# Kernel optimization log

Measured on AMD Instinct MI355X. Metric: run time of the kernel, lower is better.

## Reference

```python
import jax, jax.numpy as jnp
import numpy as np
from jax import lax

HW = 256 * 256      # patch h*w
WINDOW = 65536
STRIDE = 32768


def _conv2d(x, w, b, stride, pad):
    y = lax.conv_general_dilated(x, w, (stride, stride), [(pad, pad), (pad, pad)],
                                 dimension_numbers=('NCHW', 'OIHW', 'NCHW'))
    return y + b[None, :, None, None]


def _fcn(x, w1, b1, w2, b2, w3, b3, w4, b4):
    x = jax.nn.relu(_conv2d(x, w1, b1, 6, 6))
    x = jax.nn.relu(_conv2d(x, w2, b2, 4, 4))
    x = jax.nn.relu(_conv2d(x, w3, b3, 2, 2))
    x = jax.nn.relu(_conv2d(x, w4, b4, 1, 1))
    return x


def _avgpool2(x):
    # torch AvgPool2d(2,2,padding=1), count_include_pad=True -> sum window / 4
    s = lax.reduce_window(x, 0.0, lax.add, (1, 1, 2, 2), (1, 1, 2, 2),
                          [(0, 0), (0, 0), (1, 1), (1, 1)])
    return s * 0.25


def _cca(x, qw, qb, kw, kb, vw, vb, gamma):
    B, C, H, W = x.shape
    q = _conv2d(x, qw, qb, 1, 0)   # (B, C//8, H, W)
    k = _conv2d(x, kw, kb, 1, 0)
    v = _conv2d(x, vw, vb, 1, 0)   # (B, C, H, W)
    # column (height-axis) energies with -inf on the diagonal (self position)
    eH = jnp.einsum('bchw,bcgw->bhwg', q, k)                     # (B,H,W,H')
    eH = jnp.where(jnp.eye(H, dtype=bool)[:, None, :], -jnp.inf, eH)
    # row (width-axis) energies
    eW = jnp.einsum('bchw,bchv->bhwv', q, k)                     # (B,H,W,W')
    att = jax.nn.softmax(jnp.concatenate([eH, eW], axis=3), axis=3)
    outH = jnp.einsum('bcgw,bhwg->bchw', v, att[..., :H])
    outW = jnp.einsum('bchv,bhwv->bchw', v, att[..., H:])
    return gamma * (outH + outW) + x


def _forward(x, f0_w1, f0_b1, f0_w2, f0_b2, f0_w3, f0_b3, f0_w4, f0_b4,
             f1_w1, f1_b1, f1_w2, f1_b2, f1_w3, f1_b3, f1_w4, f1_b4,
             qw, qb, kw, kb, vw, vb, gamma, cls_w, cls_b):
    B, nc, L = x.shape
    need = HW - L % HW                 # torch pads a full extra block when L % hw == 0
    xp = jnp.pad(x, ((0, 0), (0, 0), (0, need)))
    nw = (L + need - WINDOW) // STRIDE + 1
    idx = jnp.arange(nw)[:, None] * STRIDE + jnp.arange(WINDOW)[None, :]
    wins = xp[:, 0, :][:, idx]                      # (B, nw, WINDOW) ~ torch unfold
    # torch does a raw reshape (nw,1,h,w) -> (1,1,h*w,nw); row-major reshape matches
    c_in = wins.reshape(B, 1, HW, nw)
    c0 = _fcn(c_in, f0_w1, f0_b1, f0_w2, f0_b2, f0_w3, f0_b3, f0_w4, f0_b4)
    c1 = _fcn(_avgpool2(c_in), f1_w1, f1_b1, f1_w2, f1_b2, f1_w3, f1_b3, f1_w4, f1_b4)
    a0 = _cca(c0, qw, qb, kw, kb, vw, vb, gamma)
    a1 = _cca(c1, qw, qb, kw, kb, vw, vb, gamma)   # 'twoheadfcn' reuses cca_attn0
    feat = jnp.concatenate([a0.mean(axis=(2, 3)), a1.mean(axis=(2, 3))], axis=1)
    return feat @ cls_w.T + cls_b                   # dropout = identity at eval


def setup_inputs():
    key = jax.random.key(0)
    ks = jax.random.split(key, 32)

    def he(k, shape):
        fan_in = int(np.prod(shape[1:]))
        return (jax.random.normal(k, shape) / np.sqrt(fan_in)).astype(jnp.float32)

    inp = {'x': jax.random.uniform(ks[0], (2, 1, 4194304), dtype=jnp.float32)}
    shapes = [(64, 1, 12, 12), (128, 64, 8, 8), (256, 128, 5, 5), (128, 256, 3, 3)]
    for pre, off in (('f0', 1), ('f1', 9)):
        for i, s in enumerate(shapes):
            inp[f'{pre}_w{i+1}'] = he(ks[off + 2 * i], s)
            inp[f'{pre}_b{i+1}'] = (0.01 * jax.random.normal(ks[off + 2 * i + 1], (s[0],))).astype(jnp.float32)
    inp['qw'] = he(ks[17], (16, 128, 1, 1)); inp['qb'] = jnp.zeros((16,), jnp.float32)
    inp['kw'] = he(ks[18], (16, 128, 1, 1)); inp['kb'] = jnp.zeros((16,), jnp.float32)
    inp['vw'] = he(ks[19], (128, 128, 1, 1)); inp['vb'] = jnp.zeros((128,), jnp.float32)
    inp['gamma'] = jnp.full((1,), 0.1, jnp.float32)
    inp['cls_w'] = he(ks[20], (2, 256)); inp['cls_b'] = jnp.zeros((2,), jnp.float32)
    return inp


def reference(x, f0_w1, f0_b1, f0_w2, f0_b2, f0_w3, f0_b3, f0_w4, f0_b4,
              f1_w1, f1_b1, f1_w2, f1_b2, f1_w3, f1_b3, f1_w4, f1_b4,
              qw, qb, kw, kb, vw, vb, gamma, cls_w, cls_b):
    return _forward(x, f0_w1, f0_b1, f0_w2, f0_b2, f0_w3, f0_b3, f0_w4, f0_b4,
                    f1_w1, f1_b1, f1_w2, f1_b2, f1_w3, f1_b3, f1_w4, f1_b4,
                    qw, qb, kw, kb, vw, vb, gamma, cls_w, cls_b)
```

## Files before the change

### kernel.cpp

```cpp
#include <hip/hip_runtime.h>
#include <math.h>

#define BLK 256
static const long LX = 4194304;

typedef __bf16 bf16x8 __attribute__((ext_vector_type(8)));
typedef float  f32x4  __attribute__((ext_vector_type(4)));
typedef unsigned short u16;

__device__ __forceinline__ void bf16split(float x, u16& h, u16& l) {
    unsigned u = __float_as_uint(x);
    unsigned hr = (u + 0x7fffu + ((u >> 16) & 1u)) >> 16;
    h = (u16)hr;
    float hf = __uint_as_float(hr << 16);
    float r = x - hf;
    unsigned v = __float_as_uint(r);
    unsigned lr2 = (v + 0x7fffu + ((v >> 16) & 1u)) >> 16;
    l = (u16)lr2;
}

__device__ __forceinline__ float cin_val(const float* __restrict__ x, long xbase, int h, int w) {
    if ((unsigned)h >= 65536u || (unsigned)w >= 129u) return 0.f;
    long flat = (long)h * 129 + w;
    int n = (int)(flat >> 16);
    int q = (int)(flat & 65535);
    long pos = (long)n * 32768 + q;
    return (pos < LX) ? x[xbase + pos] : 0.f;
}

__global__ __launch_bounds__(256)
void conv1_mfma_k(const float* __restrict__ x, const u16* __restrict__ wbh,
                  const u16* __restrict__ wbl, const float* __restrict__ bias,
                  u16* __restrict__ outh, u16* __restrict__ outl) {
    const long SPT = 240306;
    __shared__ u16 ph[6400];
    __shared__ u16 pl[6400];
    const int tid = threadIdx.x;
    const int b = blockIdx.y;
    const long sp0 = (long)blockIdx.x * 128;
    const long xbase = (long)b * LX;
    const int ho_min = (int)sp0 / 22;
    const int flat_start = (ho_min * 6 - 6) * 129 - 6;
    for (int i = tid; i < 6400; i += 256) {
        int flat = flat_start + i;
        float v = 0.f;
        if (flat >= 0 && flat < 65536 * 129) {
            int n = flat >> 16, q = flat & 65535;
            long pos = (long)n * 32768 + q;
            if (pos < LX) v = x[xbase + pos];
        }
        u16 h, l; bf16split(v, h, l);
        ph[i] = h; pl[i] = l;
    }
    __syncthreads();

    const int lane = tid & 63, wid = tid >> 6;
    const int lr = lane & 15;
    const int lk = (lane >> 4) << 3;

    int off0[2]; int wlo[2], whi[2];
#pragma unroll
    for (int fm = 0; fm < 2; fm++) {
        int r = (wid << 5) + (fm << 4) + lr;
        long spl = sp0 + r; if (spl >= SPT) spl = SPT - 1;
        int sp = (int)spl;
        int ho = sp / 22;
        int wo = sp - ho * 22;
        off0[fm] = (ho * 6 - 6) * 129 + (wo * 6 - 6) - flat_start;
        wlo[fm] = (wo == 0) ? 1 : 0;
        whi[fm] = (wo == 21) ? 1 : 0;
    }

    f32x4 acc[2][4];
#pragma unroll
    for (int fn = 0; fn < 4; fn++) {
        float bv = bias[(fn << 4) + lr];
#pragma unroll
        for (int fm = 0; fm < 2; fm++) { f32x4 v = {bv, bv, bv, bv}; acc[fm][fn] = v; }
    }

    const bool zhi = (lk >= 16);
#pragma unroll
    for (int c = 0; c < 5; c++) {
        bf16x8 bH[4], bL[4];
#pragma unroll
        for (int fn = 0; fn < 4; fn++) {
            int oc = (fn << 4) + lr;
            bH[fn] = *(const bf16x8*)(wbh + oc * 160 + (c << 5) + lk);
            bL[fn] = *(const bf16x8*)(wbl + oc * 160 + (c << 5) + lk);
        }
        bf16x8 aH[2], aL[2];
#pragma unroll
        for (int fm = 0; fm < 2; fm++) {
            union { bf16x8 v; u16 u[8]; } uh, ul;
            if (c == 4 && zhi) {
#pragma unroll
                for (int jj = 0; jj < 8; jj++) { uh.u[jj] = 0; ul.u[jj] = 0; }
            } else {
                int t0 = (c << 5) + lk;
                int kh0 = t0 / 12;
                int r0 = t0 - kh0 * 12;
                int jst = 12 - r0;
                int base = off0[fm] + t0 + kh0 * 117;
#pragma unroll
                for (int jj = 0; jj < 8; jj++) {
                    int wrapped = (jj >= jst) ? 1 : 0;
                    int idx = base + jj + (wrapped ? 117 : 0);
                    int kw = r0 + jj - (wrapped ? 12 : 0);
                    int bad = (wlo[fm] & ((kw < 6) ? 1 : 0)) | (whi[fm] & ((kw > 8) ? 1 : 0));
                    u16 hv = ph[idx];
                    u16 lv = pl[idx];
                    uh.u[jj] = bad ? (u16)0 : hv;
                    ul.u[jj] = bad ? (u16)0 : lv;
                }
            }
            aH[fm] = uh.v; aL[fm] = ul.v;
        }
#pragma unroll
        for (int fm = 0; fm < 2; fm++)
#pragma unroll
            for (int fn = 0; fn < 4; fn++) {
                acc[fm][fn] = __builtin_amdgcn_mfma_f32_16x16x32_bf16(aL[fm], bH[fn], acc[fm][fn], 0, 0, 0);
                acc[fm][fn] = __builtin_amdgcn_mfma_f32_16x16x32_bf16(aH[fm], bL[fn], acc[fm][fn], 0, 0, 0);
                acc[fm][fn] = __builtin_amdgcn_mfma_f32_16x16x32_bf16(aH[fm], bH[fn], acc[fm][fn], 0, 0, 0);
            }
    }
    const int row0 = (lane >> 4) << 2;
#pragma unroll
    for (int fm = 0; fm < 2; fm++) {
#pragma unroll
        for (int q = 0; q < 4; q++) {
            long sp = sp0 + (wid << 5) + (fm << 4) + row0 + q;
            if (sp < SPT) {
                long obase = ((long)b * SPT + sp) << 6;
#pragma unroll
                for (int fn = 0; fn < 4; fn++) {
                    u16 h, l;
                    bf16split(fmaxf(acc[fm][fn][q], 0.f), h, l);
                    outh[obase + (fn << 4) + lr] = h;
                    outl[obase + (fn << 4) + lr] = l;
                }
            }
        }
    }
}

__global__ __launch_bounds__(BLK)
void reorder_w1m_k(const float* __restrict__ w, u16* __restrict__ wh, u16* __restrict__ wl) {
    int t = blockIdx.x * BLK + threadIdx.x;
    if (t >= 64 * 160) return;
    int tap = t % 160, oc = t / 160;
    float v = (tap < 144) ? w[oc * 144 + tap] : 0.f;
    u16 h, l; bf16split(v, h, l);
    wh[t] = h; wl[t] = l;
}

template<int TOC>
__global__ __launch_bounds__(BLK)
void conv1_plane_k(const float* __restrict__ in, const float* __restrict__ wr1,
                   const float* __restrict__ bias, u16* __restrict__ outh, u16* __restrict__ outl,
                   int B, int Hin, int Win, int Cout, int Hout, int Wout) {
    const int K = 12, S = 6, P = 6;
    long spatial = (long)B * Hout * Wout;
    long idx = (long)blockIdx.x * BLK + threadIdx.x;
    if (idx >= spatial) return;
    int wo = (int)(idx % Wout);
    long t = idx / Wout;
    int ho = (int)(t % Hout);
    int b  = (int)(t / Hout);
    int oc0 = blockIdx.y * TOC;
    float acc[TOC];
#pragma unroll
    for (int i = 0; i < TOC; i++) acc[i] = bias[oc0 + i];
    const float* inb = in + (long)b * Hin * Win;
    int h0 = ho * S - P, w0 = wo * S - P;
    for (int kh = 0; kh < K; kh++) {
        int h = h0 + kh;
        bool hok = (unsigned)h < (unsigned)Hin;
        const float* row = inb + (long)h * Win;
        for (int kw = 0; kw < K; kw++) {
            int w = w0 + kw;
            float v = (hok && (unsigned)w < (unsigned)Win) ? row[w] : 0.f;
            const float* wp = wr1 + (kh * K + kw) * Cout + oc0;
#pragma unroll
            for (int i = 0; i < TOC; i++) acc[i] = fmaf(v, wp[i], acc[i]);
        }
    }
    u16* oph = outh + idx * Cout + oc0;
    u16* opl = outl + idx * Cout + oc0;
#pragma unroll
    for (int i4 = 0; i4 < TOC / 4; i4++) {
        u16 hx, hy, hz, hw2, la, lb, lc, ld;
        bf16split(fmaxf(acc[i4*4+0], 0.f), hx, la);
        bf16split(fmaxf(acc[i4*4+1], 0.f), hy, lb);
        bf16split(fmaxf(acc[i4*4+2], 0.f), hz, lc);
        bf16split(fmaxf(acc[i4*4+3], 0.f), hw2, ld);
        *(ushort4*)(oph + i4 * 4) = make_ushort4(hx, hy, hz, hw2);
        *(ushort4*)(opl + i4 * 4) = make_ushort4(la, lb, lc, ld);
    }
}

__global__ __launch_bounds__(BLK)
void avgpool_synth_k(const float* __restrict__ x, float* __restrict__ out, int B) {
    const int Ho = 32769, Wo = 65;
    long total = (long)B * Ho * Wo;
    long idx = (long)blockIdx.x * BLK + threadIdx.x;
    if (idx >= total) return;
    int w2 = (int)(idx % Wo);
    long t = idx / Wo;
    int p2 = (int)(t % Ho);
    int b  = (int)(t / Ho);
    long xbase = (long)b * LX;
    float s = 0.f;
#pragma unroll
    for (int dh = 0; dh < 2; dh++)
#pragma unroll
        for (int dw = 0; dw < 2; dw++)
            s += cin_val(x, xbase, 2 * p2 - 1 + dh, 2 * w2 - 1 + dw);
    out[idx] = 0.25f * s;
}

__global__ __launch_bounds__(BLK)
void reorder_w_k(const float* __restrict__ w, float* __restrict__ wrT,
                 int Cout, int Cin, int K2) {
    long total = (long)Cout * Cin * K2;
    long t = (long)blockIdx.x * BLK + threadIdx.x;
    if (t >= total) return;
    int khw = (int)(t % K2);
    long r = t / K2;
    int ic = (int)(r % Cin);
    int oc = (int)(r / Cin);
    wrT[((long)khw * Cin + ic) * Cout + oc] = w[t];
}

__global__ __launch_bounds__(BLK)
void reorder_ws_k(const float* __restrict__ w, u16* __restrict__ wh, u16* __restrict__ wl,
                  int Cout, int Cin, int Kk) {
    long total = (long)Cout * Cin * Kk * Kk;
    long t = (long)blockIdx.x * BLK + threadIdx.x;
    if (t >= total) return;
    int kw = (int)(t % Kk);
    long r = t / Kk;
    int kh = (int)(r % Kk); r /= Kk;
    int ic = (int)(r % Cin);
    int oc = (int)(r / Cin);
    long dst = (long)oc * (Cin * Kk * Kk) + (long)(kh * Kk + kw) * Cin + ic;
    u16 h, l; bf16split(w[t], h, l);
    wh[dst] = h; wl[dst] = l;
}

struct MJob {
    const u16* Ah; const u16* Al; const u16* Wh; const u16* Wl;
    const float* bias; float* out; float* part;
    int Hin, Win, Cin, cshift, Cout, K, S, P, Hout, Wout, relu, nks;
    long total; int nbx; int Ktot;
};

__global__ __launch_bounds__(256)
void mgemm2_k(MJob j0, MJob j1, int split) {
    __shared__ u16 lds[2][4][128 * 32];
    MJob j = j0;
    int bid = blockIdx.x;
    if (bid >= split) { j = j1; bid -= split; }
    const int bx = bid % j.nbx;
    int r2 = bid / j.nbx;
    const int nocb = j.Cout >> 7;
    const int ocb = (r2 % nocb) << 7;
    const int ks  = r2 / nocb;
    const int tid = threadIdx.x;
    const long spbase = (long)bx * 128;
    const int nchunk = j.Ktot >> 5;
    const int cbeg = (ks * nchunk) / j.nks;
    const int cend = ((ks + 1) * nchunk) / j.nks;

    const int sr = tid >> 1;
    const int sh = (tid & 1) << 4;
    long ssp = spbase + sr;
    const bool sval = ssp < j.total;
    long tt = sval ? ssp : 0;
    const int swo = (int)(tt % j.Wout); tt /= j.Wout;
    const int sho = (int)(tt % j.Hout);
    const int sb  = (int)(tt / j.Hout);
    const int sh0 = sho * j.S - j.P, sw0 = swo * j.S - j.P;
    const long ibase = (long)sb * j.Hin * j.Win;
    const long wbase = (long)(ocb + sr) * j.Ktot + sh;
    const int so = sr * 32 + sh;

    uint4 rA0, rA1, rL0, rL1, rB0, rB1, rM0, rM1;
    auto fetch = [&](int c) {
        int p0 = c << 5;
        int khw = p0 >> j.cshift;
        int ic0 = p0 - (khw << j.cshift);
        int kh = khw / j.K, kw = khw - kh * j.K;
        int h = sh0 + kh, w = sw0 + kw;
        bool ok = sval && (unsigned)h < (unsigned)j.Hin && (unsigned)w < (unsigned)j.Win;
        uint4 z = make_uint4(0u, 0u, 0u, 0u);
        const long e = (ibase + (long)h * j.Win + w) * j.Cin + ic0 + sh;
        rA0 = ok ? *(const uint4*)(j.Ah + e)     : z;
        rA1 = ok ? *(const uint4*)(j.Ah + e + 8) : z;
        rL0 = ok ? *(const uint4*)(j.Al + e)     : z;
        rL1 = ok ? *(const uint4*)(j.Al + e + 8) : z;
        const long we = wbase + p0;
        rB0 = *(const uint4*)(j.Wh + we);
        rB1 = *(const uint4*)(j.Wh + we + 8);
        rM0 = *(const uint4*)(j.Wl + we);
        rM1 = *(const uint4*)(j.Wl + we + 8);
    };
    auto store = [&](int buf) {
        *(uint4*)&lds[buf][0][so] = rA0; *(uint4*)&lds[buf][0][so + 8] = rA1;
        *(uint4*)&lds[buf][1][so] = rL0; *(uint4*)&lds[buf][1][so + 8] = rL1;
        *(uint4*)&lds[buf][2][so] = rB0; *(uint4*)&lds[buf][2][so + 8] = rB1;
        *(uint4*)&lds[buf][3][so] = rM0; *(uint4*)&lds[buf][3][so + 8] = rM1;
    };

    const int lane = tid & 63;
    const int wid = tid >> 6;
    const int wm = (wid >> 1) << 6, wn = (wid & 1) << 6;
    const int lr = lane & 15;
    const int lk = (lane >> 4) << 3;

    f32x4 acc[4][4];
    if (j.nks == 1) {
#pragma unroll
        for (int fn = 0; fn < 4; fn++) {
            float b = j.bias[ocb + wn + fn * 16 + lr];
#pragma unroll
            for (int fm = 0; fm < 4; fm++) { f32x4 v = {b, b, b, b}; acc[fm][fn] = v; }
        }
    } else {
#pragma unroll
        for (int fm = 0; fm < 4; fm++)
#pragma unroll
            for (int fn = 0; fn < 4; fn++) { f32x4 v = {0.f, 0.f, 0.f, 0.f}; acc[fm][fn] = v; }
    }

    fetch(cbeg); store(0);
    __syncthreads();

    for (int c = cbeg; c < cend; c++) {
        const int cur = (c - cbeg) & 1, nxt = cur ^ 1;
        const bool more = (c + 1 < cend);
        if (more) fetch(c + 1);
        const u16* Ahs = &lds[cur][0][0];
        const u16* Als = &lds[cur][1][0];
        const u16* Bhs = &lds[cur][2][0];
        const u16* Bls = &lds[cur][3][0];
        bf16x8 aH[4], aL[4], bH[4], bL[4];
#pragma unroll
        for (int f = 0; f < 4; f++) {
            aH[f] = *(const bf16x8*)(Ahs + (wm + f * 16 + lr) * 32 + lk);
            aL[f] = *(const bf16x8*)(Als + (wm + f * 16 + lr) * 32 + lk);
            bH[f] = *(const bf16x8*)(Bhs + (wn + f * 16 + lr) * 32 + lk);
            bL[f] = *(const bf16x8*)(Bls + (wn + f * 16 + lr) * 32 + lk);
        }
#pragma unroll
        for (int fm = 0; fm < 4; fm++)
#pragma unroll
            for (int fn = 0; fn < 4; fn++) {
                acc[fm][fn] = __builtin_amdgcn_mfma_f32_16x16x32_bf16(aL[fm], bH[fn], acc[fm][fn], 0, 0, 0);
                acc[fm][fn] = __builtin_amdgcn_mfma_f32_16x16x32_bf16(aH[fm], bL[fn], acc[fm][fn], 0, 0, 0);
                acc[fm][fn] = __builtin_amdgcn_mfma_f32_16x16x32_bf16(aH[fm], bH[fn], acc[fm][fn], 0, 0, 0);
            }
        if (more) store(nxt);
        __syncthreads();
    }

    const int row0 = (lane >> 4) << 2;
    if (j.nks == 1) {
#pragma unroll
        for (int fm = 0; fm < 4; fm++) {
#pragma unroll
            for (int q = 0; q < 4; q++) {
                long sp = spbase + wm + fm * 16 + row0 + q;
                if (sp < j.total) {
                    float* op = j.out + sp * j.Cout + ocb + wn + lr;
#pragma unroll
                    for (int fn = 0; fn < 4; fn++) {
                        float v = acc[fm][fn][q];
                        if (j.relu) v = fmaxf(v, 0.f);
                        op[fn * 16] = v;
                    }
                }
            }
        }
    } else {
        float* pb = j.part + ((long)ks * j.total) * j.Cout;
#pragma unroll
        for (int fm = 0; fm < 4; fm++) {
#pragma unroll
            for (int q = 0; q < 4; q++) {
                long sp = spbase + wm + fm * 16 + row0 + q;
                if (sp < j.total) {
                    float* op = pb + sp * j.Cout + ocb + wn + lr;
#pragma unroll
                    for (int fn = 0; fn < 4; fn++) op[fn * 16] = acc[fm][fn][q];
                }
            }
        }
    }
}

struct CJob {
    const float* part; const float* bias;
    float* outf; u16* outh; u16* outl;
    long n; int C; int nks; int relu;
};

__global__ __launch_bounds__(BLK)
void combine2m_k(CJob a, CJob b) {
    long q0 = a.n * (long)a.C / 4, q1 = b.n * (long)b.C / 4;
    long id = (long)blockIdx.x * BLK + threadIdx.x;
    CJob j; long f4;
    if (id < q0) { j = a; f4 = id * 4; }
    else if (id < q0 + q1) { j = b; f4 = (id - q0) * 4; }
    else return;
    long stride = j.n * (long)j.C;
    int cb = (int)(f4 % j.C);
    float4 s = *(const float4*)(j.bias + cb);
    for (int ss = 0; ss < j.nks; ss++) {
        float4 p = *(const float4*)(j.part + ss * stride + f4);
        s.x += p.x; s.y += p.y; s.z += p.z; s.w += p.w;
    }
    if (j.relu) {
        s.x = fmaxf(s.x, 0.f); s.y = fmaxf(s.y, 0.f);
        s.z = fmaxf(s.z, 0.f); s.w = fmaxf(s.w, 0.f);
    }
    if (j.outf) *(float4*)(j.outf + f4) = s;
    if (j.outh) {
        u16 hx, hy, hz, hw2, la, lb, lc, ld;
        bf16split(s.x, hx, la); bf16split(s.y, hy, lb);
        bf16split(s.z, hz, lc); bf16split(s.w, hw2, ld);
        *(ushort4*)(j.outh + f4) = make_ushort4(hx, hy, hz, hw2);
        *(ushort4*)(j.outl + f4) = make_ushort4(la, lb, lc, ld);
    }
}

__global__ __launch_bounds__(256)
void qk2_k(const float* __restrict__ in,
           const float* __restrict__ qw, const float* __restrict__ qb,
           const float* __restrict__ kw2, const float* __restrict__ kb2,
           float* __restrict__ outq, float* __restrict__ outk, long total) {
    const float* w    = blockIdx.y ? kw2 : qw;
    const float* bias = blockIdx.y ? kb2 : qb;
    float* out        = blockIdx.y ? outk : outq;
    __shared__ float As[64 * 132];
    __shared__ float Ws[128 * 16];
    int tid = threadIdx.x;
    long spbase = (long)blockIdx.x * 64;
    int r = tid >> 2;
    int cpart = (tid & 3) << 5;
    long sp = spbase + r;
    bool ok = sp < total;
    const float* ip = in + sp * 128 + cpart;
#pragma unroll
    for (int jj = 0; jj < 8; jj++) {
        float4 v = ok ? *(const float4*)(ip + jj * 4) : make_float4(0.f, 0.f, 0.f, 0.f);
        *(float4*)&As[r * 132 + cpart + jj * 4] = v;
    }
    for (int t = tid; t < 2048; t += 256) Ws[(t & 127) * 16 + (t >> 7)] = w[t];
    __syncthreads();
    int ocp = (tid & 3) << 2;
    float acc[4] = {bias[ocp], bias[ocp + 1], bias[ocp + 2], bias[ocp + 3]};
    for (int ic = 0; ic < 128; ic++) {
        float a = As[r * 132 + ic];
#pragma unroll
        for (int jj = 0; jj < 4; jj++) acc[jj] = fmaf(a, Ws[ic * 16 + ocp + jj], acc[jj]);
    }
    if (ok) {
#pragma unroll
        for (int jj = 0; jj < 4; jj++) out[sp * 16 + ocp + jj] = acc[jj];
    }
}

struct AJob {
    const float* q; const float* kk; const float* v;
    float* pacc; float* pm; float* pl;
    int B, H, W, nrt, ns, ntile;
};

__global__ __launch_bounds__(256)
void cca_part_k(AJob j0, AJob j1, int n0) {
    const int RT = 16, TG = 64;
    __shared__ float lbuf[8192];
    __shared__ float mlb2[32];
    float* kls    = lbuf;
    float* sc     = lbuf + 1088;
    float* scales = lbuf + 2176;
    AJob j = j0;
    int bid = blockIdx.x;
    if (bid >= n0) { j = j1; bid -= n0; }
    int rt = bid % j.nrt; int t = bid / j.nrt;
    int ksp = t % j.ns; t /= j.ns;
    int w = t % j.W; int b = t / j.W;
    const int H = j.H, W = j.W;
    const int tid = threadIdx.x;
    const int r = tid >> 4, l16 = tid & 15;
    const int h = rt * RT + r;
    const int hc = (h < H) ? h : (H - 1);
    const long colbase = (long)b * H * W + w;
    const long rowbase = ((long)b * H + hc) * W;

    float qreg[16];
    {
        const float* qp = j.q + (rowbase + w) * 16;
#pragma unroll
        for (int jj = 0; jj < 4; jj++) {
            float4 t4 = *(const float4*)(qp + 4 * jj);
            qreg[4*jj] = t4.x; qreg[4*jj+1] = t4.y; qreg[4*jj+2] = t4.z; qreg[4*jj+3] = t4.w;
        }
    }
    const int lane6 = tid & 63;
    const int wid = tid >> 6;
    const int c2 = lane6 << 1;
    float accv[16][2];
#pragma unroll
    for (int i = 0; i < 16; i++) { accv[i][0] = 0.f; accv[i][1] = 0.f; }

    float m = -INFINITY, l = 0.f;
    const int gp = l16 * 4;

    const int tbeg = (ksp * j.ntile) / j.ns;
    const int tend = ((ksp + 1) * j.ntile) / j.ns;
    for (int tt2 = tbeg; tt2 < tend; tt2++) {
        const int g0 = tt2 * TG;
        {
            int kr = tid >> 2, kc = (tid & 3) << 2;
            int gg = g0 + kr;
            float4 kv = make_float4(0.f, 0.f, 0.f, 0.f);
            if (gg < H) kv = *(const float4*)(j.kk + (colbase + (long)gg * W) * 16 + kc);
            kls[kr * 17 + kc + 0] = kv.x; kls[kr * 17 + kc + 1] = kv.y;
            kls[kr * 17 + kc + 2] = kv.z; kls[kr * 17 + kc + 3] = kv.w;
        }
        __syncthreads();
        float sloc[4];
#pragma unroll
        for (int i = 0; i < 4; i++) {
            int gg = g0 + gp + i;
            float d = 0.f;
#pragma unroll
            for (int c = 0; c < 16; c++) d = fmaf(qreg[c], kls[(gp + i) * 17 + c], d);
            sloc[i] = (gg >= H || gg == h) ? -INFINITY : d;
        }
        float tmax = fmaxf(fmaxf(sloc[0], sloc[1]), fmaxf(sloc[2], sloc[3]));
#pragma unroll
        for (int off = 1; off < 16; off <<= 1) tmax = fmaxf(tmax, __shfl_xor(tmax, off, 16));
        float mt = fmaxf(m, tmax);
        float scale = __expf(m - mt);
        float ps = 0.f;
#pragma unroll
        for (int i = 0; i < 4; i++) {
            float p = __expf(sloc[i] - mt);
            ps += p;
            sc[r * 68 + gp + i] = p;
        }
#pragma unroll
        for (int off = 1; off < 16; off <<= 1) ps += __shfl_xor(ps, off, 16);
        l = l * scale + ps;
        m = mt;
        if (l16 == 0) scales[r] = scale;
        __syncthreads();
        {
            float4 sA = *(const float4*)&scales[0];
            float4 sB = *(const float4*)&scales[4];
            float4 sC = *(const float4*)&scales[8];
            float4 sD = *(const float4*)&scales[12];
            float sarr[16] = {sA.x,sA.y,sA.z,sA.w, sB.x,sB.y,sB.z,sB.w,
                              sC.x,sC.y,sC.z,sC.w, sD.x,sD.y,sD.z,sD.w};
#pragma unroll
            for (int row = 0; row < 16; row++) {
                accv[row][0] *= sarr[row];
                accv[row][1] *= sarr[row];
            }
#pragma unroll
            for (int s = 0; s < 2; s++) {
                const int k0 = (wid << 4) + (s << 3);
                float2 v2[8];
#pragma unroll
                for (int kq = 0; kq < 8; kq++) {
                    int gg = g0 + k0 + kq;
                    if (gg >= H) gg = H - 1;
                    v2[kq] = *(const float2*)(j.v + (colbase + (long)gg * W) * 128 + c2);
                }
#pragma unroll
                for (int row = 0; row < 16; row++) {
                    float4 pA = *(const float4*)&sc[row * 68 + k0];
                    float4 pB = *(const float4*)&sc[row * 68 + k0 + 4];
                    accv[row][0] = fmaf(pA.x, v2[0].x, accv[row][0]);
                    accv[row][1] = fmaf(pA.x, v2[0].y, accv[row][1]);
                    accv[row][0] = fmaf(pA.y, v2[1].x, accv[row][0]);
                    accv[row][1] = fmaf(pA.y, v2[1].y, accv[row][1]);
                    accv[row][0] = fmaf(pA.z, v2[2].x, accv[row][0]);
                    accv[row][1] = fmaf(pA.z, v2[2].y, accv[row][1]);
                    accv[row][0] = fmaf(pA.w, v2[3].x, accv[row][0]);
                    accv[row][1] = fmaf(pA.w, v2[3].y, accv[row][1]);
                    accv[row][0] = fmaf(pB.x, v2[4].x, accv[row][0]);
                    accv[row][1] = fmaf(pB.x, v2[4].y, accv[row][1]);
                    accv[row][0] = fmaf(pB.y, v2[5].x, accv[row][0]);
                    accv[row][1] = fmaf(pB.y, v2[5].y, accv[row][1]);
                    accv[row][0] = fmaf(pB.z, v2[6].x, accv[row][0]);
                    accv[row][1] = fmaf(pB.z, v2[6].y, accv[row][1]);
                    accv[row][0] = fmaf(pB.w, v2[7].x, accv[row][0]);
                    accv[row][1] = fmaf(pB.w, v2[7].y, accv[row][1]);
                }
            }
        }
        __syncthreads();
    }
    if (ksp == 0) {
        float sw[3];
        float twmax = -INFINITY;
#pragma unroll
        for (int jj = 0; jj < 3; jj++) {
            sw[jj] = -INFINITY;
            if (jj < W) {
                const float* kp = j.kk + (rowbase + jj) * 16;
                float d = 0.f;
#pragma unroll
                for (int c = 0; c < 16; c++) d = fmaf(qreg[c], kp[c], d);
                sw[jj] = d;
                twmax = fmaxf(twmax, d);
            }
        }
        float mt = fmaxf(m, twmax);
        float scale = __expf(m - mt);
        l *= scale;
#pragma unroll
        for (int jj = 0; jj < 3; jj++) {
            if (jj < W) {
                float p = __expf(sw[jj] - mt);
                l += p;
                if (l16 == 0) sc[r * 68 + jj] = p;
            }
        }
        m = mt;
        if (l16 == 0) scales[r] = scale;
    }
    if (l16 == 0) { mlb2[2 * r] = m; mlb2[2 * r + 1] = l; }
    __syncthreads();
    if (ksp == 0) {
        float4 sA = *(const float4*)&scales[0];
        float4 sB = *(const float4*)&scales[4];
        float4 sC = *(const float4*)&scales[8];
        float4 sD = *(const float4*)&scales[12];
        float sarr[16] = {sA.x,sA.y,sA.z,sA.w, sB.x,sB.y,sB.z,sB.w,
                          sC.x,sC.y,sC.z,sC.w, sD.x,sD.y,sD.z,sD.w};
#pragma unroll
        for (int row = 0; row < 16; row++) {
            accv[row][0] *= sarr[row];
            accv[row][1] *= sarr[row];
            int hr = rt * RT + row;
            int hcr = (hr < H) ? hr : (H - 1);
            long rb = ((long)b * H + hcr) * W;
#pragma unroll
            for (int jj = 0; jj < 3; jj++) {
                if (jj < W) {
                    float p = sc[row * 68 + jj];
                    float2 vv = *(const float2*)(j.v + (rb + jj) * 128 + c2);
                    accv[row][0] = fmaf(p, vv.x, accv[row][0]);
                    accv[row][1] = fmaf(p, vv.y, accv[row][1]);
                }
            }
        }
    }
    __syncthreads();
#pragma unroll
    for (int row = 0; row < 16; row++) {
        *(float2*)&lbuf[(wid << 11) + (row << 7) + c2] = make_float2(accv[row][0], accv[row][1]);
    }
    __syncthreads();
    {
        int orow = tid >> 4, ocb = (tid & 15) << 3;
        int hr = rt * RT + orow;
        if (hr < H) {
            float4 r0 = make_float4(0.f, 0.f, 0.f, 0.f);
            float4 r1 = make_float4(0.f, 0.f, 0.f, 0.f);
#pragma unroll
            for (int wv = 0; wv < 4; wv++) {
                float4 a0 = *(const float4*)&lbuf[(wv << 11) + (orow << 7) + ocb];
                float4 a1 = *(const float4*)&lbuf[(wv << 11) + (orow << 7) + ocb + 4];
                r0.x += a0.x; r0.y += a0.y; r0.z += a0.z; r0.w += a0.w;
                r1.x += a1.x; r1.y += a1.y; r1.z += a1.z; r1.w += a1.w;
            }
            long qi = ((long)b * H + hr) * W + w;
            float* pp = j.pacc + (qi * j.ns + ksp) * 128 + ocb;
            *(float4*)pp       = r0;
            *(float4*)(pp + 4) = r1;
            if ((tid & 15) == 0) {
                j.pm[qi * j.ns + ksp] = mlb2[2 * orow];
                j.pl[qi * j.ns + ksp] = mlb2[2 * orow + 1];
            }
        }
    }
}

struct CCJob {
    const float* x; const float* pacc; const float* pm; const float* pl;
    float* out; long rows; int ns;
};

__global__ __launch_bounds__(BLK)
void cca_comb_k(CCJob a, CCJob b, const float* __restrict__ gamma) {
    long q0 = a.rows * 32, q1 = b.rows * 32;
    long id = (long)blockIdx.x * BLK + threadIdx.x;
    CCJob j; long lid;
    if (id < q0) { j = a; lid = id; }
    else if (id < q0 + q1) { j = b; lid = id - q0; }
    else return;
    long qi = lid >> 5;
    int c4 = (int)(lid & 31) << 2;
    int ns = j.ns;
    float M = -INFINITY;
    for (int s = 0; s < ns; s++) M = fmaxf(M, j.pm[qi * ns + s]);
    float L = 0.f;
    float4 acc = make_float4(0.f, 0.f, 0.f, 0.f);
    for (int s = 0; s < ns; s++) {
        float wgt = __expf(j.pm[qi * ns + s] - M);
        L += j.pl[qi * ns + s] * wgt;
        float4 p = *(const float4*)(j.pacc + (qi * ns + s) * 128 + c4);
        acc.x = fmaf(wgt, p.x, acc.x); acc.y = fmaf(wgt, p.y, acc.y);
        acc.z = fmaf(wgt, p.z, acc.z); acc.w = fmaf(wgt, p.w, acc.w);
    }
    float g = gamma[0] / L;
    float4 xr = *(const float4*)(j.x + qi * 128 + c4);
    float4 o = make_float4(g * acc.x + xr.x, g * acc.y + xr.y,
                           g * acc.z + xr.z, g * acc.w + xr.w);
    *(float4*)(j.out + qi * 128 + c4) = o;
}

__global__ __launch_bounds__(BLK)
void mean_part_k(const float* __restrict__ a, float* __restrict__ part, int HW, int NS) {
    int bx = blockIdx.x;
    int b = bx / NS, sc_ = bx % NS;
    int tid = threadIdx.x;
    int c = tid & 127, half = tid >> 7;
    int per = (HW + NS - 1) / NS;
    int s0 = sc_ * per, s1 = s0 + per; if (s1 > HW) s1 = HW;
    float acc = 0.f;
    for (int s = s0 + half; s < s1; s += 2) acc += a[((long)b * HW + s) * 128 + c];
    __shared__ float red[BLK];
    red[tid] = acc; __syncthreads();
    if (half == 0) part[(long)bx * 128 + c] = red[c] + red[c + 128];
}

__global__ __launch_bounds__(BLK)
void final2_k(const float* __restrict__ part0, const float* __restrict__ part1, int NS,
              const float* __restrict__ w, const float* __restrict__ bias,
              float* __restrict__ out, float hw0, float hw1) {
    __shared__ float feat[512];
    int tid = threadIdx.x;
    for (int t = tid; t < 512; t += BLK) {
        int b = t >> 8, c = t & 255;
        float s = 0.f;
        if (c < 128) {
            for (int ns = 0; ns < NS; ns++) s += part0[((long)b * NS + ns) * 128 + c];
            s /= hw0;
        } else {
            int cc = c - 128;
            for (int ns = 0; ns < NS; ns++) s += part1[((long)b * NS + ns) * 128 + cc];
            s /= hw1;
        }
        feat[t] = s;
    }
    __syncthreads();
    if (tid < 4) {
        int b = tid >> 1, jj = tid & 1;
        float s = bias[jj];
        for (int c = 0; c < 256; c++) s += feat[b * 256 + c] * w[jj * 256 + c];
        out[b * 2 + jj] = s;
    }
}

static inline long cdiv(long a, long b) { return (a + b - 1) / b; }

extern "C" void kernel_launch(void* const* d_in, const int* in_sizes, int n_in,
                              void* d_out, int out_size, void* d_ws, size_t ws_size,
                              hipStream_t stream) {
    const float* x     = (const float*)d_in[0];
    const float* f0w1  = (const float*)d_in[1];
    const float* f0b1  = (const float*)d_in[2];
    const float* f0w2  = (const float*)d_in[3];
    const float* f0b2  = (const float*)d_in[4];
    const float* f0w3  = (const float*)d_in[5];
    const float* f0b3  = (const float*)d_in[6];
    const float* f0w4  = (const float*)d_in[7];
    const float* f0b4  = (const float*)d_in[8];
    const float* f1w1  = (const float*)d_in[9];
    const float* f1b1  = (const float*)d_in[10];
    const float* f1w2  = (const float*)d_in[11];
    const float* f1b2  = (const float*)d_in[12];
    const float* f1w3  = (const float*)d_in[13];
    const float* f1b3  = (const float*)d_in[14];
    const float* f1w4  = (const float*)d_in[15];
    const float* f1b4  = (const float*)d_in[16];
    const float* qw    = (const float*)d_in[17];
    const float* qb    = (const float*)d_in[18];
    const float* kw    = (const float*)d_in[19];
    const float* kb    = (const float*)d_in[20];
    const float* vw    = (const float*)d_in[21];
    const float* vb    = (const float*)d_in[22];
    const float* gamma = (const float*)d_in[23];
    const float* clsw  = (const float*)d_in[24];
    const float* clsb  = (const float*)d_in[25];
    float* ws = (float*)d_ws;
    float* outp = (float*)d_out;

    const int B = 2;
    size_t off = 0;
    auto alloc = [&](size_t nfl) { size_t o = off; off += (nfl + 63) & ~(size_t)63; return o; };
    size_t o_pool = alloc((size_t)B * 32769 * 65);
    size_t o_A0h  = alloc((size_t)B * 10923 * 22 * 32);
    size_t o_A0l  = alloc((size_t)B * 10923 * 22 * 32);
    size_t o_A1h  = alloc((size_t)B * 5462 * 11 * 32);
    size_t o_A1l  = alloc((size_t)B * 5462 * 11 * 32);
    size_t o_B0h  = alloc((size_t)B * 2731 * 6 * 64);
    size_t o_B0l  = alloc((size_t)B * 2731 * 6 * 64);
    size_t o_c0   = alloc((size_t)B * 1366 * 3 * 128);
    size_t o_c1   = alloc((size_t)B * 683 * 2 * 128);
    size_t o_w1r1 = alloc((size_t)144 * 64);
    size_t o_w1mh = alloc((size_t)64 * 160 / 2);
    size_t o_w1ml = alloc((size_t)64 * 160 / 2);
    size_t o_w2h0 = alloc((size_t)128 * 4096 / 2);
    size_t o_w2l0 = alloc((size_t)128 * 4096 / 2);
    size_t o_w2h1 = alloc((size_t)128 * 4096 / 2);
    size_t o_w2l1 = alloc((size_t)128 * 4096 / 2);
    size_t o_w3h0 = alloc((size_t)256 * 3200 / 2);
    size_t o_w3l0 = alloc((size_t)256 * 3200 / 2);
    size_t o_w3h1 = alloc((size_t)256 * 3200 / 2);
    size_t o_w3l1 = alloc((size_t)256 * 3200 / 2);
    size_t o_w4h0 = alloc((size_t)128 * 2304 / 2);
    size_t o_w4l0 = alloc((size_t)128 * 2304 / 2);
    size_t o_w4h1 = alloc((size_t)128 * 2304 / 2);
    size_t o_w4l1 = alloc((size_t)128 * 2304 / 2);
    size_t o_wvh  = alloc((size_t)128 * 128 / 2);
    size_t o_wvl  = alloc((size_t)128 * 128 / 2);
    size_t o_part = alloc((size_t)2 * (32772 + 8196) * 128);
    size_t need_main = off;
    size_t o_B1h = o_pool;
    size_t o_B1l = o_pool + (size_t)B * 1366 * 3 * 64;
    size_t sub = o_A0h;
    auto salloc = [&](size_t nfl) { size_t o = sub; sub += (nfl + 63) & ~(size_t)63; return o; };
    size_t o_C0h = salloc((size_t)B * 1366 * 3 * 128);
    size_t o_C0l = salloc((size_t)B * 1366 * 3 * 128);
    size_t o_C1h = salloc((size_t)B * 683 * 2 * 128);
    size_t o_C1l = salloc((size_t)B * 683 * 2 * 128);
    size_t o_c0h = salloc((size_t)B * 1366 * 3 * 64);
    size_t o_c0l = salloc((size_t)B * 1366 * 3 * 64);
    size_t o_c1h = salloc((size_t)B * 683 * 2 * 64);
    size_t o_c1l = salloc((size_t)B * 683 * 2 * 64);
    size_t o_q0  = salloc((size_t)B * 1366 * 3 * 16);
    size_t o_k0  = salloc((size_t)B * 1366 * 3 * 16);
    size_t o_v0  = salloc((size_t)B * 1366 * 3 * 128);
    size_t o_a0  = salloc((size_t)B * 1366 * 3 * 128);
    size_t o_q1  = salloc((size_t)B * 683 * 2 * 16);
    size_t o_k1  = salloc((size_t)B * 683 * 2 * 16);
    size_t o_v1  = salloc((size_t)B * 683 * 2 * 128);
    size_t o_a1  = salloc((size_t)B * 683 * 2 * 128);
    size_t o_p0  = salloc((size_t)B * 8 * 128);
    size_t o_p1  = salloc((size_t)B * 8 * 128);
    if (ws_size < need_main * sizeof(float)) {
        hipMemsetAsync(d_out, 0, (size_t)out_size * sizeof(float), stream);
        return;
    }
    auto U16 = [&](size_t o) { return (u16*)(ws + o); };

    {
        long tot = (long)B * 32769 * 65;
        avgpool_synth_k<<<dim3(cdiv(tot, BLK)), BLK, 0, stream>>>(x, ws + o_pool, B);
    }
    reorder_w_k<<<dim3(cdiv((long)64 * 144, BLK)), BLK, 0, stream>>>(f1w1, ws + o_w1r1, 64, 1, 144);
    reorder_w1m_k<<<dim3(cdiv((long)64 * 160, BLK)), BLK, 0, stream>>>(f0w1, U16(o_w1mh), U16(o_w1ml));
    reorder_ws_k<<<dim3(cdiv((long)128 * 64 * 64, BLK)), BLK, 0, stream>>>(f0w2, U16(o_w2h0), U16(o_w2l0), 128, 64, 8);
    reorder_ws_k<<<dim3(cdiv((long)128 * 64 * 64, BLK)), BLK, 0, stream>>>(f1w2, U16(o_w2h1), U16(o_w2l1), 128, 64, 8);
    reorder_ws_k<<<dim3(cdiv((long)256 * 128 * 25, BLK)), BLK, 0, stream>>>(f0w3, U16(o_w3h0), U16(o_w3l0), 256, 128, 5);
    reorder_ws_k<<<dim3(cdiv((long)256 * 128 * 25, BLK)), BLK, 0, stream>>>(f1w3, U16(o_w3h1), U16(o_w3l1), 256, 128, 5);
    reorder_ws_k<<<dim3(cdiv((long)128 * 256 * 9, BLK)), BLK, 0, stream>>>(f0w4, U16(o_w4h0), U16(o_w4l0), 128, 256, 3);
    reorder_ws_k<<<dim3(cdiv((long)128 * 256 * 9, BLK)), BLK, 0, stream>>>(f1w4, U16(o_w4h1), U16(o_w4l1), 128, 256, 3);
    reorder_ws_k<<<dim3(cdiv((long)128 * 128, BLK)), BLK, 0, stream>>>(vw, U16(o_wvh), U16(o_wvl), 128, 128, 1);
    {
        long sp = (long)B * 5462 * 11;
        conv1_plane_k<32><<<dim3(cdiv(sp, BLK), 2), BLK, 0, stream>>>(
            ws + o_pool, ws + o_w1r1, f1b1, U16(o_A1h), U16(o_A1l), B, 32769, 65, 64, 5462, 11);
    }
    {
        int nbx = (int)cdiv(240306L, 128);
        conv1_mfma_k<<<dim3(nbx, B), 256, 0, stream>>>(
            x, U16(o_w1mh), U16(o_w1ml), f0b1, U16(o_A0h), U16(o_A0l));
    }

    float* partp = ws + o_part;
    auto mkM = [&](size_t ah, size_t al, size_t wh, size_t wl, const float* bias, float* out,
                   int Hin, int Win, int Cin, int cshift, int Cout,
                   int K, int S, int P, int Hout, int Wout, int relu) {
        MJob g;
        g.Ah = U16(ah); g.Al = U16(al); g.Wh = U16(wh); g.Wl = U16(wl);
        g.bias = bias; g.out = out; g.part = nullptr;
        g.Hin = Hin; g.Win = Win; g.Cin = Cin; g.cshift = cshift; g.Cout = Cout;
        g.K = K; g.S = S; g.P = P; g.Hout = Hout; g.Wout = Wout; g.relu = relu; g.nks = 1;
        g.total = (long)B * Hout * Wout;
        g.nbx = (int)((g.total + 127) / 128);
        g.Ktot = K * K * Cin;
        return g;
    };
    auto launchM = [&](MJob a, MJob b, int nks) {
        a.nks = nks; b.nks = nks;
        a.part = partp;
        b.part = partp + (size_t)nks * a.total * a.Cout;
        int na = a.nbx * (a.Cout >> 7) * nks;
        int nb = b.nbx * (b.Cout >> 7) * nks;
        mgemm2_k<<<dim3(na + nb), 256, 0, stream>>>(a, b, na);
    };

    {
        MJob a = mkM(o_A0h, o_A0l, o_w2h0, o_w2l0, f0b2, nullptr, 10923, 22, 64, 6, 128, 8, 4, 4, 2731, 6, 1);
        MJob b = mkM(o_A1h, o_A1l, o_w2h1, o_w2l1, f1b2, nullptr, 5462, 11, 64, 6, 128, 8, 4, 4, 1366, 3, 1);
        launchM(a, b, 2);
        CJob ca = {partp, f0b2, nullptr, U16(o_B0h), U16(o_B0l), a.total, 128, 2, 1};
        CJob cb = {partp + (size_t)2 * a.total * 128, f1b2, nullptr, U16(o_B1h), U16(o_B1l), b.total, 128, 2, 1};
        long n4 = (a.total * 128 + b.total * 128) / 4;
        combine2m_k<<<dim3(cdiv(n4, BLK)), BLK, 0, stream>>>(ca, cb);
    }
    {
        MJob a = mkM(o_B0h, o_B0l, o_w3h0, o_w3l0, f0b3, nullptr, 2731, 6, 128, 7, 256, 5, 2, 2, 1366, 3, 1);
        MJob b = mkM(o_B1h, o_B1l, o_w3h1, o_w3l1, f1b3, nullptr, 1366, 3, 128, 7, 256, 5, 2, 2, 683, 2, 1);
        launchM(a, b, 3);
        CJob ca = {partp, f0b3, nullptr, U16(o_C0h), U16(o_C0l), a.total, 256, 3, 1};
        CJob cb = {partp + (size_t)3 * a.total * 256, f1b3, nullptr, U16(o_C1h), U16(o_C1l), b.total, 256, 3, 1};
        long n4 = (a.total * 256 + b.total * 256) / 4;
        combine2m_k<<<dim3(cdiv(n4, BLK)), BLK, 0, stream>>>(ca, cb);
    }
    {
        MJob a = mkM(o_C0h, o_C0l, o_w4h0, o_w4l0, f0b4, nullptr, 1366, 3, 256, 8, 128, 3, 1, 1, 1366, 3, 1);
        MJob b = mkM(o_C1h, o_C1l, o_w4h1, o_w4l1, f1b4, nullptr, 683, 2, 256, 8, 128, 3, 1, 1, 683, 2, 1);
        launchM(a, b, 6);
        CJob ca = {partp, f0b4, ws + o_c0, U16(o_c0h), U16(o_c0l), a.total, 128, 6, 1};
        CJob cb = {partp + (size_t)6 * a.total * 128, f1b4, ws + o_c1, U16(o_c1h), U16(o_c1l), b.total, 128, 6, 1};
        long n4 = (a.total * 128 + b.total * 128) / 4;
        combine2m_k<<<dim3(cdiv(n4, BLK)), BLK, 0, stream>>>(ca, cb);
    }
    {
        long tot0 = (long)B * 1366 * 3;
        qk2_k<<<dim3(cdiv(tot0, 64), 2), 256, 0, stream>>>(
            ws + o_c0, qw, qb, kw, kb, ws + o_q0, ws + o_k0, tot0);
        long tot1 = (long)B * 683 * 2;
        qk2_k<<<dim3(cdiv(tot1, 64), 2), 256, 0, stream>>>(
            ws + o_c1, qw, qb, kw, kb, ws + o_q1, ws + o_k1, tot1);
    }
    {
        MJob a = mkM(o_c0h, o_c0l, o_wvh, o_wvl, vb, ws + o_v0, 1366, 3, 128, 7, 128, 1, 1, 0, 1366, 3, 0);
        MJob b = mkM(o_c1h, o_c1l, o_wvh, o_wvl, vb, ws + o_v1, 683, 2, 128, 7, 128, 1, 1, 0, 683, 2, 0);
        launchM(a, b, 1);
    }
    {
        const int nrt0 = 86, nrt1 = 43;
        const int ns0 = 6, ns1 = 3;
        const long rows0 = (long)B * 1366 * 3;
        const long rows1 = (long)B * 683 * 2;
        size_t pp = o_part;
        auto palloc = [&](size_t nfl) { size_t o = pp; pp += (nfl + 63) & ~(size_t)63; return o; };
        size_t o_pa0 = palloc((size_t)rows0 * ns0 * 128);
        size_t o_pm0 = palloc((size_t)rows0 * ns0);
        size_t o_pl0 = palloc((size_t)rows0 * ns0);
        size_t o_pa1 = palloc((size_t)rows1 * ns1 * 128);
        size_t o_pm1 = palloc((size_t)rows1 * ns1);
        size_t o_pl1 = palloc((size_t)rows1 * ns1);
        AJob a0 = { ws + o_q0, ws + o_k0, ws + o_v0,
                    ws + o_pa0, ws + o_pm0, ws + o_pl0, B, 1366, 3, nrt0, ns0, 22 };
        AJob a1 = { ws + o_q1, ws + o_k1, ws + o_v1,
                    ws + o_pa1, ws + o_pm1, ws + o_pl1, B, 683, 2, nrt1, ns1, 11 };
        int n0 = B * 3 * nrt0 * ns0;
        int n1 = B * 2 * nrt1 * ns1;
        cca_part_k<<<dim3(n0 + n1), 256, 0, stream>>>(a0, a1, n0);
        CCJob c0 = { ws + o_c0, ws + o_pa0, ws + o_pm0, ws + o_pl0, ws + o_a0, rows0, ns0 };
        CCJob c1 = { ws + o_c1, ws + o_pa1, ws + o_pm1, ws + o_pl1, ws + o_a1, rows1, ns1 };
        long tot = (rows0 + rows1) * 32;
        cca_comb_k<<<dim3(cdiv(tot, BLK)), BLK, 0, stream>>>(c0, c1, gamma);
    }
    mean_part_k<<<dim3(B * 8), BLK, 0, stream>>>(ws + o_a0, ws + o_p0, 1366 * 3, 8);
    mean_part_k<<<dim3(B * 8), BLK, 0, stream>>>(ws + o_a1, ws + o_p1, 683 * 2, 8);
    final2_k<<<dim3(1), BLK, 0, stream>>>(ws + o_p0, ws + o_p1, 8, clsw, clsb, outp,
                                          (float)(1366 * 3), (float)(683 * 2));
}
```

Before: 748.5 us.

## Move pooled-branch conv1 to MFMA and stream GEMM weights from global

Replaces the scalar FP32 first convolution of the pooled branch with an MFMA kernel. The kernel stages a strip of the pooled input into LDS as bf16 hi/lo pairs and uses split-bf16 products, reusing the padded weight layout of the other conv1. Separately, the shared GEMM kernel no longer stages weight tiles in LDS. Each wave loads its B fragments straight from global memory, which halves LDS usage and cuts LDS traffic but relies on cache hits for weight reuse across waves.

```diff
diff --git a/kernel.cpp b/kernel.cpp
--- a/kernel.cpp
+++ b/kernel.cpp
@@ -145,6 +145,119 @@
     }
 }
 
+__global__ __launch_bounds__(256)
+void conv1p_mfma_k(const float* __restrict__ pool, const u16* __restrict__ wbh,
+                   const u16* __restrict__ wbl, const float* __restrict__ bias,
+                   u16* __restrict__ outh, u16* __restrict__ outl) {
+    const int SPT = 60082;
+    const int HWP = 32769 * 65;
+    __shared__ u16 ph[5504];
+    __shared__ u16 pl[5504];
+    const int tid = threadIdx.x;
+    const int b = blockIdx.y;
+    const long sp0 = (long)blockIdx.x * 128;
+    const float* pb = pool + (long)b * HWP;
+    const int ho_min = (int)sp0 / 11;
+    const int fs = (ho_min * 6 - 6) * 65 - 6;
+    for (int i = tid; i < 5504; i += 256) {
+        int flat = fs + i;
+        float v = (flat >= 0 && flat < HWP) ? pb[flat] : 0.f;
+        u16 h, l; bf16split(v, h, l);
+        ph[i] = h; pl[i] = l;
+    }
+    __syncthreads();
+
+    const int lane = tid & 63, wid = tid >> 6;
+    const int lr = lane & 15;
+    const int lk = (lane >> 4) << 3;
+
+    int off0[2]; int wlo[2], whi[2];
+#pragma unroll
+    for (int fm = 0; fm < 2; fm++) {
+        int r = (wid << 5) + (fm << 4) + lr;
+        long spl = sp0 + r; if (spl >= SPT) spl = SPT - 1;
+        int sp = (int)spl;
+        int ho = sp / 11;
+        int wo = sp - ho * 11;
+        off0[fm] = (ho - ho_min) * 390 + wo * 6;
+        wlo[fm] = (wo == 0) ? 1 : 0;
+        whi[fm] = (wo == 10) ? 1 : 0;
+    }
+
+    f32x4 acc[2][4];
+#pragma unroll
+    for (int fn = 0; fn < 4; fn++) {
+        float bv = bias[(fn << 4) + lr];
+#pragma unroll
+        for (int fm = 0; fm < 2; fm++) { f32x4 v = {bv, bv, bv, bv}; acc[fm][fn] = v; }
+    }
+
+    const bool zhi = (lk >= 16);
+#pragma unroll
+    for (int c = 0; c < 5; c++) {
+        bf16x8 bH[4], bL[4];
+#pragma unroll
+        for (int fn = 0; fn < 4; fn++) {
+            int oc = (fn << 4) + lr;
+            bH[fn] = *(const bf16x8*)(wbh + oc * 160 + (c << 5) + lk);
+            bL[fn] = *(const bf16x8*)(wbl + oc * 160 + (c << 5) + lk);
+        }
+        bf16x8 aH[2], aL[2];
+#pragma unroll
+        for (int fm = 0; fm < 2; fm++) {
+            union { bf16x8 v; u16 u[8]; } uh, ul;
+            if (c == 4 && zhi) {
+#pragma unroll
+                for (int jj = 0; jj < 8; jj++) { uh.u[jj] = 0; ul.u[jj] = 0; }
+            } else {
+                int t0 = (c << 5) + lk;
+                int kh0 = t0 / 12;
+                int r0 = t0 - kh0 * 12;
+                int jst = 12 - r0;
+                int base = off0[fm] + kh0 * 65 + r0;
+#pragma unroll
+                for (int jj = 0; jj < 8; jj++) {
+                    int wrapped = (jj >= jst) ? 1 : 0;
+                    int idx = base + jj + (wrapped ? 53 : 0);
+                    int kw = r0 + jj - (wrapped ? 12 : 0);
+                    int bad = (wlo[fm] & ((kw < 6) ? 1 : 0)) | (whi[fm] & ((kw > 10) ? 1 : 0));
+                    u16 hv = ph[idx];
+                    u16 lv = pl[idx];
+                    uh.u[jj] = bad ? (u16)0 : hv;
+                    ul.u[jj] = bad ? (u16)0 : lv;
+                }
+            }
+            aH[fm] = uh.v; aL[fm] = ul.v;
+        }
+#pragma unroll
+        for (int fm = 0; fm < 2; fm++)
+#pragma unroll
+            for (int fn = 0; fn < 4; fn++) {
+                acc[fm][fn] = __builtin_amdgcn_mfma_f32_16x16x32_bf16(aL[fm], bH[fn], acc[fm][fn], 0, 0, 0);
+                acc[fm][fn] = __builtin_amdgcn_mfma_f32_16x16x32_bf16(aH[fm], bL[fn], acc[fm][fn], 0, 0, 0);
+                acc[fm][fn] = __builtin_amdgcn_mfma_f32_16x16x32_bf16(aH[fm], bH[fn], acc[fm][fn], 0, 0, 0);
+            }
+    }
+    const int row0 = (lane >> 4) << 2;
+#pragma unroll
+    for (int fm = 0; fm < 2; fm++) {
+#pragma unroll
+        for (int q = 0; q < 4; q++) {
+            long sp = sp0 + (wid << 5) + (fm << 4) + row0 + q;
+            if (sp < SPT) {
+                long obase = ((long)b * SPT + sp) << 6;
+#pragma unroll
+                for (int fn = 0; fn < 4; fn++) {
+                    u16 h, l;
+                    bf16split(fmaxf(acc[fm][fn][q], 0.f), h, l);
+                    outh[obase + (fn << 4) + lr] = h;
+                    outl[obase + (fn << 4) + lr] = l;
+                }
+            }
+        }
+    }
+}
+
 __global__ __launch_bounds__(BLK)
 void reorder_w1m_k(const float* __restrict__ w, u16* __restrict__ wh, u16* __restrict__ wl) {
     int t = blockIdx.x * BLK + threadIdx.x;
@@ -153,51 +266,6 @@
     float v = (tap < 144) ? w[oc * 144 + tap] : 0.f;
     u16 h, l; bf16split(v, h, l);
     wh[t] = h; wl[t] = l;
-}
-
-template<int TOC>
-__global__ __launch_bounds__(BLK)
-void conv1_plane_k(const float* __restrict__ in, const float* __restrict__ wr1,
-                   const float* __restrict__ bias, u16* __restrict__ outh, u16* __restrict__ outl,
-                   int B, int Hin, int Win, int Cout, int Hout, int Wout) {
-    const int K = 12, S = 6, P = 6;
-    long spatial = (long)B * Hout * Wout;
-    long idx = (long)blockIdx.x * BLK + threadIdx.x;
-    if (idx >= spatial) return;
-    int wo = (int)(idx % Wout);
-    long t = idx / Wout;
-    int ho = (int)(t % Hout);
-    int b  = (int)(t / Hout);
-    int oc0 = blockIdx.y * TOC;
-    float acc[TOC];
-#pragma unroll
-    for (int i = 0; i < TOC; i++) acc[i] = bias[oc0 + i];
-    const float* inb = in + (long)b * Hin * Win;
-    int h0 = ho * S - P, w0 = wo * S - P;
-    for (int kh = 0; kh < K; kh++) {
-        int h = h0 + kh;
-        bool hok = (unsigned)h < (unsigned)Hin;
-        const float* row = inb + (long)h * Win;
-        for (int kw = 0; kw < K; kw++) {
-            int w = w0 + kw;
-            float v = (hok && (unsigned)w < (unsigned)Win) ? row[w] : 0.f;
-            const float* wp = wr1 + (kh * K + kw) * Cout + oc0;
-#pragma unroll
-            for (int i = 0; i < TOC; i++) acc[i] = fmaf(v, wp[i], acc[i]);
-        }
-    }
-    u16* oph = outh + idx * Cout + oc0;
-    u16* opl = outl + idx * Cout + oc0;
-#pragma unroll
-    for (int i4 = 0; i4 < TOC / 4; i4++) {
-        u16 hx, hy, hz, hw2, la, lb, lc, ld;
-        bf16split(fmaxf(acc[i4*4+0], 0.f), hx, la);
-        bf16split(fmaxf(acc[i4*4+1], 0.f), hy, lb);
-        bf16split(fmaxf(acc[i4*4+2], 0.f), hz, lc);
-        bf16split(fmaxf(acc[i4*4+3], 0.f), hw2, ld);
-        *(ushort4*)(oph + i4 * 4) = make_ushort4(hx, hy, hz, hw2);
-        *(ushort4*)(opl + i4 * 4) = make_ushort4(la, lb, lc, ld);
-    }
 }
 
 __global__ __launch_bounds__(BLK)
@@ -218,19 +286,6 @@
         for (int dw = 0; dw < 2; dw++)
             s += cin_val(x, xbase, 2 * p2 - 1 + dh, 2 * w2 - 1 + dw);
     out[idx] = 0.25f * s;
-}
-
-__global__ __launch_bounds__(BLK)
-void reorder_w_k(const float* __restrict__ w, float* __restrict__ wrT,
-                 int Cout, int Cin, int K2) {
-    long total = (long)Cout * Cin * K2;
-    long t = (long)blockIdx.x * BLK + threadIdx.x;
-    if (t >= total) return;
-    int khw = (int)(t % K2);
-    long r = t / K2;
-    int ic = (int)(r % Cin);
-    int oc = (int)(r / Cin);
-    wrT[((long)khw * Cin + ic) * Cout + oc] = w[t];
 }
 
 __global__ __launch_bounds__(BLK)
@@ -258,7 +313,7 @@
 
 __global__ __launch_bounds__(256)
 void mgemm2_k(MJob j0, MJob j1, int split) {
-    __shared__ u16 lds[2][4][128 * 32];
+    __shared__ u16 lds[2][2][128 * 32];
     MJob j = j0;
     int bid = blockIdx.x;
     if (bid >= split) { j = j1; bid -= split; }
@@ -283,11 +338,10 @@
     const int sb  = (int)(tt / j.Hout);
     const int sh0 = sho * j.S - j.P, sw0 = swo * j.S - j.P;
     const long ibase = (long)sb * j.Hin * j.Win;
-    const long wbase = (long)(ocb + sr) * j.Ktot + sh;
     const int so = sr * 32 + sh;
 
-    uint4 rA0, rA1, rL0, rL1, rB0, rB1, rM0, rM1;
-    auto fetch = [&](int c) {
+    uint4 rA0, rA1, rL0, rL1;
+    auto fetchA = [&](int c) {
         int p0 = c << 5;
         int khw = p0 >> j.cshift;
         int ic0 = p0 - (khw << j.cshift);
@@ -300,17 +354,10 @@
         rA1 = ok ? *(const uint4*)(j.Ah + e + 8) : z;
         rL0 = ok ? *(const uint4*)(j.Al + e)     : z;
         rL1 = ok ? *(const uint4*)(j.Al + e + 8) : z;
-        const long we = wbase + p0;
-        rB0 = *(const uint4*)(j.Wh + we);
-        rB1 = *(const uint4*)(j.Wh + we + 8);
-        rM0 = *(const uint4*)(j.Wl + we);
-        rM1 = *(const uint4*)(j.Wl + we + 8);
     };
-    auto store = [&](int buf) {
+    auto storeA = [&](int buf) {
         *(uint4*)&lds[buf][0][so] = rA0; *(uint4*)&lds[buf][0][so + 8] = rA1;
         *(uint4*)&lds[buf][1][so] = rL0; *(uint4*)&lds[buf][1][so + 8] = rL1;
-        *(uint4*)&lds[buf][2][so] = rB0; *(uint4*)&lds[buf][2][so + 8] = rB1;
-        *(uint4*)&lds[buf][3][so] = rM0; *(uint4*)&lds[buf][3][so + 8] = rM1;
     };
 
     const int lane = tid & 63;
@@ -318,6 +365,7 @@
     const int wm = (wid >> 1) << 6, wn = (wid & 1) << 6;
     const int lr = lane & 15;
     const int lk = (lane >> 4) << 3;
+    const long wrow = (long)(ocb + wn + lr) * j.Ktot + lk;
 
     f32x4 acc[4][4];
     if (j.nks == 1) {
@@ -334,24 +382,27 @@
             for (int fn = 0; fn < 4; fn++) { f32x4 v = {0.f, 0.f, 0.f, 0.f}; acc[fm][fn] = v; }
     }
 
-    fetch(cbeg); store(0);
+    fetchA(cbeg); storeA(0);
     __syncthreads();
 
     for (int c = cbeg; c < cend; c++) {
         const int cur = (c - cbeg) & 1, nxt = cur ^ 1;
         const bool more = (c + 1 < cend);
-        if (more) fetch(c + 1);
+        if (more) fetchA(c + 1);
+        bf16x8 bH[4], bL[4];
+#pragma unroll
+        for (int fn = 0; fn < 4; fn++) {
+            const long wo2 = wrow + (long)fn * 16 * j.Ktot + (c << 5);
+            bH[fn] = *(const bf16x8*)(j.Wh + wo2);
+            bL[fn] = *(const bf16x8*)(j.Wl + wo2);
+        }
         const u16* Ahs = &lds[cur][0][0];
         const u16* Als = &lds[cur][1][0];
-        const u16* Bhs = &lds[cur][2][0];
-        const u16* Bls = &lds[cur][3][0];
-        bf16x8 aH[4], aL[4], bH[4], bL[4];
+        bf16x8 aH[4], aL[4];
 #pragma unroll
         for (int f = 0; f < 4; f++) {
             aH[f] = *(const bf16x8*)(Ahs + (wm + f * 16 + lr) * 32 + lk);
             aL[f] = *(const bf16x8*)(Als + (wm + f * 16 + lr) * 32 + lk);
-            bH[f] = *(const bf16x8*)(Bhs + (wn + f * 16 + lr) * 32 + lk);
-            bL[f] = *(const bf16x8*)(Bls + (wn + f * 16 + lr) * 32 + lk);
         }
 #pragma unroll
         for (int fm = 0; fm < 4; fm++)
@@ -361,7 +412,7 @@
                 acc[fm][fn] = __builtin_amdgcn_mfma_f32_16x16x32_bf16(aH[fm], bL[fn], acc[fm][fn], 0, 0, 0);
                 acc[fm][fn] = __builtin_amdgcn_mfma_f32_16x16x32_bf16(aH[fm], bH[fn], acc[fm][fn], 0, 0, 0);
             }
-        if (more) store(nxt);
+        if (more) storeA(nxt);
         __syncthreads();
     }
 
@@ -816,9 +867,10 @@
     size_t o_B0l  = alloc((size_t)B * 2731 * 6 * 64);
     size_t o_c0   = alloc((size_t)B * 1366 * 3 * 128);
     size_t o_c1   = alloc((size_t)B * 683 * 2 * 128);
-    size_t o_w1r1 = alloc((size_t)144 * 64);
     size_t o_w1mh = alloc((size_t)64 * 160 / 2);
     size_t o_w1ml = alloc((size_t)64 * 160 / 2);
+    size_t o_w1nh = alloc((size_t)64 * 160 / 2);
+    size_t o_w1nl = alloc((size_t)64 * 160 / 2);
     size_t o_w2h0 = alloc((size_t)128 * 4096 / 2);
     size_t o_w2l0 = alloc((size_t)128 * 4096 / 2);
     size_t o_w2h1 = alloc((size_t)128 * 4096 / 2);
@@ -867,8 +919,8 @@
         long tot = (long)B * 32769 * 65;
         avgpool_synth_k<<<dim3(cdiv(tot, BLK)), BLK, 0, stream>>>(x, ws + o_pool, B);
     }
-    reorder_w_k<<<dim3(cdiv((long)64 * 144, BLK)), BLK, 0, stream>>>(f1w1, ws + o_w1r1, 64, 1, 144);
     reorder_w1m_k<<<dim3(cdiv((long)64 * 160, BLK)), BLK, 0, stream>>>(f0w1, U16(o_w1mh), U16(o_w1ml));
+    reorder_w1m_k<<<dim3(cdiv((long)64 * 160, BLK)), BLK, 0, stream>>>(f1w1, U16(o_w1nh), U16(o_w1nl));
     reorder_ws_k<<<dim3(cdiv((long)128 * 64 * 64, BLK)), BLK, 0, stream>>>(f0w2, U16(o_w2h0), U16(o_w2l0), 128, 64, 8);
     reorder_ws_k<<<dim3(cdiv((long)128 * 64 * 64, BLK)), BLK, 0, stream>>>(f1w2, U16(o_w2h1), U16(o_w2l1), 128, 64, 8);
     reorder_ws_k<<<dim3(cdiv((long)256 * 128 * 25, BLK)), BLK, 0, stream>>>(f0w3, U16(o_w3h0), U16(o_w3l0), 256, 128, 5);
@@ -877,9 +929,9 @@
     reorder_ws_k<<<dim3(cdiv((long)128 * 256 * 9, BLK)), BLK, 0, stream>>>(f1w4, U16(o_w4h1), U16(o_w4l1), 128, 256, 3);
     reorder_ws_k<<<dim3(cdiv((long)128 * 128, BLK)), BLK, 0, stream>>>(vw, U16(o_wvh), U16(o_wvl), 128, 128, 1);
     {
-        long sp = (long)B * 5462 * 11;
-        conv1_plane_k<32><<<dim3(cdiv(sp, BLK), 2), BLK, 0, stream>>>(
-            ws + o_pool, ws + o_w1r1, f1b1, U16(o_A1h), U16(o_A1l), B, 32769, 65, 64, 5462, 11);
+        int nbx = (int)cdiv(60082L, 128);
+        conv1p_mfma_k<<<dim3(nbx, B), 256, 0, stream>>>(
+            ws + o_pool, U16(o_w1nh), U16(o_w1nl), f1b1, U16(o_A1h), U16(o_A1l));
     }
     {
         int nbx = (int)cdiv(240306L, 128);
```

After: 890.1 us. +18.9%, slower.
